# Optimization experiments

Hardware: AMD Instinct MI355X
Metric: run time of the kernel (lower is better)

## Reference

```python
import jax, jax.numpy as jnp
import numpy as np

B, S, K = 256, 50, 8
D, NH, NL = 512, 8, 2
N_KNOWS, N_PROBS = 1000, 20000
L2 = 2 * NL  # forward layers then backward layers, stacked
HD = D // NH
NEG = -1e9


def _ln(x, g, b, eps=1e-5):
    mu = x.mean(-1, keepdims=True)
    v = ((x - mu) ** 2).mean(-1, keepdims=True)
    return (x - mu) * jax.lax.rsqrt(v + eps) * g + b


def _block(x, m, Wq, bq, Wk, bk, Wv, bv, g1, be1, W1, b1, W2, b2, g2, be2):
    # x: [3B,S,D], m: [3B,1,S,S] additive-OR mask (True = blocked)
    Bx, Sx, Dx = x.shape
    Q = (x @ Wq + bq).reshape(Bx, Sx, NH, HD)
    Kt = (x @ Wk + bk).reshape(Bx, Sx, NH, HD)
    V = (x @ Wv + bv).reshape(Bx, Sx, NH, HD)
    a = jnp.einsum('bqnh,bknh->bnqk', Q, Kt) * (HD ** -0.5)
    a = jnp.where(m, NEG, a)
    p = jax.nn.softmax(a, axis=-1)
    p = jnp.where(m, 0.0, p)  # masked_fill + softmax + where, as in torch source
    o = jnp.einsum('bnqk,bknh->bqnh', p, V).reshape(Bx, Sx, Dx)
    x = _ln(x + o, g1, be1)
    h = jnp.maximum(x @ W1 + b1, 0.0) @ W2 + b2
    return _ln(x + h, g2, be2)


def _forward(probs_his, knows_his, corrs_his, knows_tab, probs_tab, types_tab, pos_tab,
             Wq, bq, Wk, bk, Wv, bv, g1, be1, W1, b1, W2, b2, g2, be2,
             pW1, pb1, pW2, pb2, pW3, pb3):
    info = knows_tab[knows_his].sum(-2) + probs_tab[probs_his] + pos_tab[jnp.arange(S)][None]
    c = corrs_his
    right_t = jnp.where(c, 1, 2)   # corrs==False -> 2
    wrong_t = jnp.where(c, 2, 0)   # corrs==True  -> 2
    norm_t = c.astype(jnp.int32)
    # fold the 3 counterfactual passes (right / wrong / normal) into the batch dim
    x3 = jnp.concatenate([info + types_tab[right_t], info + types_tab[wrong_t], info + types_tab[norm_t]], 0)
    kpm = jnp.tile(probs_his == 0, (3, 1))               # key padding mask [3B,S]
    km = kpm[:, :, None] | kpm[:, None, :]               # OR-combined [3B,S,S]
    tri = jnp.triu(jnp.ones((S, S), bool), 1)
    fm = (tri[None] | km)[:, None]                       # forward (causal) mask
    bm = (tri.T[None] | km)[:, None]                     # backward (anti-causal) mask
    f = x3
    b = x3
    for i in range(NL):
        f = _block(f, fm, Wq[i], bq[i], Wk[i], bk[i], Wv[i], bv[i], g1[i], be1[i], W1[i], b1[i], W2[i], b2[i], g2[i], be2[i])
    for i in range(NL, L2):
        b = _block(b, bm, Wq[i], bq[i], Wk[i], bk[i], Wv[i], bv[i], g1[i], be1[i], W1[i], b1[i], W2[i], b2[i], g2[i], be2[i])
    out = jnp.concatenate([b[:, :1], f[:, :-2] + b[:, 2:], f[:, -1:]], 1)
    h = jnp.concatenate([out, jnp.tile(info, (3, 1, 1))], -1)
    h = jnp.maximum(h @ pW1 + pb1, 0.0)
    h = jnp.maximum(h @ pW2 + pb2, 0.0)
    sc = jax.nn.sigmoid((h @ pW3 + pb3)[..., 0]).reshape(3, B, S)
    # zero out padded positions instead of ragged boolean gather (fixed shape, jit-safe)
    return jnp.where((probs_his > 0)[None], sc, 0.0)


def setup_inputs() -> dict:
    key = jax.random.key(0)
    ks = jax.random.split(key, 16)
    sc = 0.02
    d = {}
    d['probs_his'] = jax.random.randint(ks[0], (B, S), 0, N_PROBS)
    d['knows_his'] = jax.random.randint(ks[1], (B, S, K), 0, N_KNOWS + 1)
    d['corrs_his'] = jax.random.randint(ks[2], (B, S), 0, 2).astype(bool)
    d['knows_tab'] = (jax.random.normal(ks[3], (N_KNOWS + 1, D)) * sc).at[0].set(0.0)  # padding_idx=0
    d['probs_tab'] = (jax.random.normal(ks[4], (N_PROBS + 1, D)) * sc).at[0].set(0.0)
    d['types_tab'] = jax.random.normal(ks[5], (3, D)) * sc
    d['pos_tab'] = jax.random.normal(ks[6], (50, D)) * sc
    d['Wq'] = jax.random.normal(ks[7], (L2, D, D)) * sc
    d['Wk'] = jax.random.normal(ks[8], (L2, D, D)) * sc
    d['Wv'] = jax.random.normal(ks[9], (L2, D, D)) * sc
    d['W1'] = jax.random.normal(ks[10], (L2, D, D)) * sc
    d['W2'] = jax.random.normal(ks[11], (L2, D, D)) * sc
    for n in ('bq', 'bk', 'bv', 'b1', 'b2', 'be1', 'be2'):
        d[n] = jnp.zeros((L2, D))
    d['g1'] = jnp.ones((L2, D))
    d['g2'] = jnp.ones((L2, D))
    d['pW1'] = jax.random.normal(ks[12], (2 * D, D)) * sc
    d['pb1'] = jnp.zeros((D,))
    d['pW2'] = jax.random.normal(ks[13], (D, D // 2)) * sc
    d['pb2'] = jnp.zeros((D // 2,))
    d['pW3'] = jax.random.normal(ks[14], (D // 2, 1)) * sc
    d['pb3'] = jnp.zeros((1,))
    return d


def reference(probs_his, knows_his, corrs_his, knows_tab, probs_tab, types_tab, pos_tab,
              Wq, bq, Wk, bk, Wv, bv, g1, be1, W1, b1, W2, b2, g2, be2,
              pW1, pb1, pW2, pb2, pW3, pb3):
    return _forward(probs_his, knows_his, corrs_his, knows_tab, probs_tab, types_tab, pos_tab,
                    Wq, bq, Wk, bk, Wv, bv, g1, be1, W1, b1, W2, b2, g2, be2,
                    pW1, pb1, pW2, pb2, pW3, pb3)
```

## Files before the change

### kernel.cpp

```cpp
#include <hip/hip_runtime.h>
#include <hip/hip_bf16.h>

#define SEQ 50
#define DD  512
#define NHD 8
#define HDIM 64
#define MPROWS 38400
#define MTROWS 76800

typedef __hip_bfloat16 bf;
typedef __attribute__((ext_vector_type(8))) short bf16x8;
typedef __attribute__((ext_vector_type(4))) float f32x4;

__device__ __forceinline__ float bf2f(unsigned short u) {
    unsigned int x = ((unsigned int)u) << 16;
    return __builtin_bit_cast(float, x);
}
__device__ __forceinline__ unsigned short f2bu(float f) {
    unsigned int u = __builtin_bit_cast(unsigned int, f);
    u += 0x7fffu + ((u >> 16) & 1u);
    return (unsigned short)(u >> 16);
}

#define ASYNC16(g, l) __builtin_amdgcn_global_load_lds( \
    (__attribute__((address_space(1))) void*)(g),       \
    (__attribute__((address_space(3))) void*)(l), 16, 0, 0)

__global__ __launch_bounds__(256) void transpose_cast(
    const float* __restrict__ src, bf* __restrict__ dst,
    int R, int C, size_t sStride, size_t dStride)
{
    __shared__ float tile[32][33];
    int l = blockIdx.z;
    src += (size_t)l * sStride;
    dst += (size_t)l * dStride;
    int c0 = blockIdx.x * 32, r0 = blockIdx.y * 32;
    int tx = threadIdx.x & 31, ty = threadIdx.x >> 5;
    for (int i = ty; i < 32; i += 8)
        tile[i][tx] = src[(size_t)(r0 + i) * C + c0 + tx];
    __syncthreads();
    for (int i = ty; i < 32; i += 8)
        dst[(size_t)(c0 + i) * R + r0 + tx] = __float2bfloat16(tile[tx][i]);
}

__global__ __launch_bounds__(256) void biascat_kernel(
    const float* __restrict__ bq, const float* __restrict__ bk,
    const float* __restrict__ bv, float* __restrict__ out)
{
    int i = blockIdx.x * 256 + threadIdx.x;
    if (i >= 4 * 1536) return;
    int l = i / 1536, c = i % 1536;
    float v;
    if (c < 512)       v = bq[l * 512 + c];
    else if (c < 1024) v = bk[l * 512 + c - 512];
    else               v = bv[l * 512 + c - 1024];
    out[i] = v;
}

__global__ __launch_bounds__(256) void tproj_kernel(
    const float* __restrict__ types_tab, const bf* __restrict__ WTqkv,
    bf* __restrict__ Tt)
{
    int gid = blockIdx.x * 256 + threadIdx.x;
    if (gid >= 9216) return;
    int hl = gid / 4608;
    int t  = (gid / 1536) % 3;
    int n  = gid % 1536;
    const unsigned short* w =
        (const unsigned short*)(WTqkv + (size_t)(hl * 2) * 786432 + (size_t)n * 512);
    const float* ty = types_tab + t * 512;
    float a = 0.f;
    for (int k = 0; k < 512; ++k) a += ty[k] * bf2f(w[k]);
    Tt[gid] = __float2bfloat16(a);
}

__global__ __launch_bounds__(256) void embed_kernel(
    const int* __restrict__ probs_his, const int* __restrict__ knows_his,
    const int* __restrict__ corrs, const float* __restrict__ knows_tab,
    const float* __restrict__ probs_tab, const float* __restrict__ types_tab,
    const float* __restrict__ pos_tab, bf* __restrict__ info, bf* __restrict__ X)
{
    int bs = blockIdx.x * 4 + (threadIdx.x >> 6);
    int lane = threadIdx.x & 63;
    int s = bs % SEQ;
    int p = probs_his[bs];
    int c = corrs[bs];
    int d0 = lane * 8;

    float v[8];
    #pragma unroll
    for (int j = 0; j < 8; ++j)
        v[j] = probs_tab[(size_t)p * DD + d0 + j] + pos_tab[(size_t)s * DD + d0 + j];
    for (int k = 0; k < 8; ++k) {
        int ki = knows_his[bs * 8 + k];
        const float* kr = knows_tab + (size_t)ki * DD + d0;
        #pragma unroll
        for (int j = 0; j < 8; ++j) v[j] += kr[j];
    }
    int t0 = c ? 1 : 2;
    int t1 = c ? 2 : 0;
    int t2 = c ? 1 : 0;
    const float* T0 = types_tab + t0 * DD + d0;
    const float* T1 = types_tab + t1 * DD + d0;
    const float* T2 = types_tab + t2 * DD + d0;
    uint4 xi, x0, x1, x2;
    unsigned short* pi = (unsigned short*)&xi;
    unsigned short* p0 = (unsigned short*)&x0;
    unsigned short* p1 = (unsigned short*)&x1;
    unsigned short* p2 = (unsigned short*)&x2;
    #pragma unroll
    for (int j = 0; j < 8; ++j) {
        pi[j] = f2bu(v[j]);
        p0[j] = f2bu(v[j] + T0[j]);
        p1[j] = f2bu(v[j] + T1[j]);
        p2[j] = f2bu(v[j] + T2[j]);
    }
    size_t base = (size_t)bs * DD + d0;
    const size_t PB = (size_t)12800 * DD;
    *(uint4*)(info + base) = xi;
    *(uint4*)(X + 0 * PB + base) = x0;
    *(uint4*)(X + 1 * PB + base) = x1;
    *(uint4*)(X + 2 * PB + base) = x2;
    *(uint4*)(X + 3 * PB + base) = x0;
    *(uint4*)(X + 4 * PB + base) = x1;
    *(uint4*)(X + 5 * PB + base) = x2;
}

template <int RELU>
__global__ __launch_bounds__(256) void gemm_bt(
    const bf* __restrict__ Ap, const bf* __restrict__ WT0, const bf* __restrict__ WT1,
    const float* __restrict__ bias0, const float* __restrict__ bias1,
    bf* __restrict__ Cp, int N, int Kd, int nN, int mtHalf)
{
    __shared__ bf Al[128 * 64];
    __shared__ bf Bl[128 * 64];
    int nwg = gridDim.x;
    int f = blockIdx.x;
    int q8 = nwg >> 3, r8 = nwg & 7;
    int xcd = f & 7, pos = f >> 3;
    int e = (xcd < r8 ? xcd * (q8 + 1) : r8 * (q8 + 1) + (xcd - r8) * q8) + pos;
    int bm = e / nN, bn = e - bm * nN;
    const bf* WTp;
    const float* bias;
    if (bm < mtHalf) { WTp = WT0; bias = bias0; }
    else             { WTp = WT1; bias = bias1; }
    int m0 = bm * 128, n0 = bn * 128;
    int t = threadIdx.x, lane = t & 63, wave = t >> 6;
    int wr = wave >> 1, wc = wave & 1;
    int lr = lane & 15, lg = lane >> 4;

    f32x4 acc[4][4];
    #pragma unroll
    for (int m = 0; m < 4; ++m)
        #pragma unroll
        for (int n = 0; n < 4; ++n)
            acc[m][n] = (f32x4){0.f, 0.f, 0.f, 0.f};

    for (int kt = 0; kt < Kd; kt += 64) {
        #pragma unroll
        for (int i = 0; i < 4; ++i) {
            int c = i * 256 + t;
            int row = c >> 3, col = (c & 7) * 8;
            ASYNC16(Ap  + (size_t)(m0 + row) * Kd + kt + col, Al + c * 8);
            ASYNC16(WTp + (size_t)(n0 + row) * Kd + kt + col, Bl + c * 8);
        }
        __syncthreads();
        #pragma unroll
        for (int kk = 0; kk < 64; kk += 32) {
            int ko = kk + lg * 8;
            bf16x8 af[4], bfr[4];
            #pragma unroll
            for (int m = 0; m < 4; ++m)
                af[m] = *(const bf16x8*)(Al + (wr * 64 + m * 16 + lr) * 64 + ko);
            #pragma unroll
            for (int n = 0; n < 4; ++n)
                bfr[n] = *(const bf16x8*)(Bl + (wc * 64 + n * 16 + lr) * 64 + ko);
            #pragma unroll
            for (int m = 0; m < 4; ++m)
                #pragma unroll
                for (int n = 0; n < 4; ++n)
                    acc[m][n] = __builtin_amdgcn_mfma_f32_16x16x32_bf16(af[m], bfr[n], acc[m][n], 0, 0, 0);
        }
        __syncthreads();
    }
    unsigned short* Cs = (unsigned short*)Cp;
    #pragma unroll
    for (int n = 0; n < 4; ++n) {
        int col = n0 + wc * 64 + n * 16 + lr;
        float bvv = bias[col];
        #pragma unroll
        for (int m = 0; m < 4; ++m) {
            #pragma unroll
            for (int r = 0; r < 4; ++r) {
                int row = m0 + wr * 64 + m * 16 + lg * 4 + r;
                float v = acc[m][n][r] + bvv;
                if (RELU) v = fmaxf(v, 0.f);
                Cs[(size_t)row * N + col] = f2bu(v);
            }
        }
    }
}

__global__ __launch_bounds__(256) void gemm_l0(
    const bf* __restrict__ Ap, const bf* __restrict__ WTp,
    const float* __restrict__ bias, const bf* __restrict__ Tth,
    const int* __restrict__ corrs, bf* __restrict__ QKVc)
{
    __shared__ bf Al[128 * 64];
    __shared__ bf Bl[128 * 64];
    const int nN = 12, Kd = 512, N = 1536;
    int nwg = gridDim.x;
    int f = blockIdx.x;
    int q8 = nwg >> 3, r8 = nwg & 7;
    int xcd = f & 7, pos = f >> 3;
    int e = (xcd < r8 ? xcd * (q8 + 1) : r8 * (q8 + 1) + (xcd - r8) * q8) + pos;
    int bm = e / nN, bn = e - bm * nN;
    int m0 = bm * 128, n0 = bn * 128;
    int t = threadIdx.x, lane = t & 63, wave = t >> 6;
    int wr = wave >> 1, wc = wave & 1;
    int lr = lane & 15, lg = lane >> 4;

    f32x4 acc[4][4];
    #pragma unroll
    for (int m = 0; m < 4; ++m)
        #pragma unroll
        for (int n = 0; n < 4; ++n)
            acc[m][n] = (f32x4){0.f, 0.f, 0.f, 0.f};

    for (int kt = 0; kt < Kd; kt += 64) {
        #pragma unroll
        for (int i = 0; i < 4; ++i) {
            int c = i * 256 + t;
            int row = c >> 3, col = (c & 7) * 8;
            ASYNC16(Ap  + (size_t)(m0 + row) * Kd + kt + col, Al + c * 8);
            ASYNC16(WTp + (size_t)(n0 + row) * Kd + kt + col, Bl + c * 8);
        }
        __syncthreads();
        #pragma unroll
        for (int kk = 0; kk < 64; kk += 32) {
            int ko = kk + lg * 8;
            bf16x8 af[4], bfr[4];
            #pragma unroll
            for (int m = 0; m < 4; ++m)
                af[m] = *(const bf16x8*)(Al + (wr * 64 + m * 16 + lr) * 64 + ko);
            #pragma unroll
            for (int n = 0; n < 4; ++n)
                bfr[n] = *(const bf16x8*)(Bl + (wc * 64 + n * 16 + lr) * 64 + ko);
            #pragma unroll
            for (int m = 0; m < 4; ++m)
                #pragma unroll
                for (int n = 0; n < 4; ++n)
                    acc[m][n] = __builtin_amdgcn_mfma_f32_16x16x32_bf16(af[m], bfr[n], acc[m][n], 0, 0, 0);
        }
        __syncthreads();
    }
    unsigned short* Cs = (unsigned short*)QKVc;
    const unsigned short* Tu = (const unsigned short*)Tth;
    #pragma unroll
    for (int n = 0; n < 4; ++n) {
        int col = n0 + wc * 64 + n * 16 + lr;
        float bvv = bias[col];
        float T0c = bf2f(Tu[0 * 1536 + col]);
        float T1c = bf2f(Tu[1 * 1536 + col]);
        float T2c = bf2f(Tu[2 * 1536 + col]);
        #pragma unroll
        for (int m = 0; m < 4; ++m) {
            #pragma unroll
            for (int r = 0; r < 4; ++r) {
                int row = m0 + wr * 64 + m * 16 + lg * 4 + r;
                int c = corrs[row];
                float v = acc[m][n][r] + bvv;
                float tv0 = c ? T1c : T2c;
                float tv1 = c ? T2c : T0c;
                float tv2 = c ? T1c : T0c;
                size_t b0 = (size_t)row * N + col;
                Cs[b0]                         = f2bu(v + tv0);
                Cs[b0 + (size_t)12800 * N]     = f2bu(v + tv1);
                Cs[b0 + (size_t)25600 * N]     = f2bu(v + tv2);
            }
        }
    }
}

__global__ __launch_bounds__(256) void gemm_head(
    const bf* __restrict__ Ap, const bf* __restrict__ WTp,
    const bf* __restrict__ IPp, bf* __restrict__ Cp, int nN)
{
    __shared__ bf Al[128 * 64];
    __shared__ bf Bl[128 * 64];
    const int Kd = 512, N = 512;
    int nwg = gridDim.x;
    int f = blockIdx.x;
    int q8 = nwg >> 3, r8 = nwg & 7;
    int xcd = f & 7, pos = f >> 3;
    int e = (xcd < r8 ? xcd * (q8 + 1) : r8 * (q8 + 1) + (xcd - r8) * q8) + pos;
    int bm = e / nN, bn = e - bm * nN;
    int m0 = bm * 128, n0 = bn * 128;
    int t = threadIdx.x, lane = t & 63, wave = t >> 6;
    int wr = wave >> 1, wc = wave & 1;
    int lr = lane & 15, lg = lane >> 4;

    f32x4 acc[4][4];
    #pragma unroll
    for (int m = 0; m < 4; ++m)
        #pragma unroll
        for (int n = 0; n < 4; ++n)
            acc[m][n] = (f32x4){0.f, 0.f, 0.f, 0.f};

    for (int kt = 0; kt < Kd; kt += 64) {
        #pragma unroll
        for (int i = 0; i < 4; ++i) {
            int c = i * 256 + t;
            int row = c >> 3, col = (c & 7) * 8;
            ASYNC16(Ap  + (size_t)(m0 + row) * Kd + kt + col, Al + c * 8);
            ASYNC16(WTp + (size_t)(n0 + row) * Kd + kt + col, Bl + c * 8);
        }
        __syncthreads();
        #pragma unroll
        for (int kk = 0; kk < 64; kk += 32) {
            int ko = kk + lg * 8;
            bf16x8 af[4], bfr[4];
            #pragma unroll
            for (int m = 0; m < 4; ++m)
                af[m] = *(const bf16x8*)(Al + (wr * 64 + m * 16 + lr) * 64 + ko);
            #pragma unroll
            for (int n = 0; n < 4; ++n)
                bfr[n] = *(const bf16x8*)(Bl + (wc * 64 + n * 16 + lr) * 64 + ko);
            #pragma unroll
            for (int m = 0; m < 4; ++m)
                #pragma unroll
                for (int n = 0; n < 4; ++n)
                    acc[m][n] = __builtin_amdgcn_mfma_f32_16x16x32_bf16(af[m], bfr[n], acc[m][n], 0, 0, 0);
        }
        __syncthreads();
    }
    unsigned short* Cs = (unsigned short*)Cp;
    const unsigned short* IPu = (const unsigned short*)IPp;
    #pragma unroll
    for (int n = 0; n < 4; ++n) {
        int col = n0 + wc * 64 + n * 16 + lr;
        #pragma unroll
        for (int m = 0; m < 4; ++m) {
            #pragma unroll
            for (int r = 0; r < 4; ++r) {
                int row = m0 + wr * 64 + m * 16 + lg * 4 + r;
                int rr = row % 12800;
                float v = acc[m][n][r] + bf2f(IPu[(size_t)rr * 512 + col]);
                v = fmaxf(v, 0.f);
                Cs[(size_t)row * N + col] = f2bu(v);
            }
        }
    }
}

__global__ __launch_bounds__(128, 2) void attn_mfma(
    const bf* __restrict__ QKVc, const int* __restrict__ probs_his,
    bf* __restrict__ Oc, int seq0)
{
    __shared__ bf Pl_s[2][4096];
    __shared__ bf Vt_s[2][4096];
    int wave = threadIdx.x >> 6, lane = threadIdx.x & 63;
    bf* Pl = Pl_s[wave];
    bf* Vt = Vt_s[wave];
    int task = blockIdx.x * 2 + wave;
    int h = task & 7, seqL = task >> 3;
    int seqG = seq0 + seqL;
    int st = seqG / 768, b = seqG % 256;
    int lr = lane & 15, kg = lane >> 4;
    const bf* Qb = QKVc + (size_t)seqL * SEQ * 1536 + h * HDIM;
    const bf* Kb = Qb + 512;
    const bf* Vb = Qb + 1024;

    int pvv = (lane < SEQ) ? probs_his[b * SEQ + lane] : 1;
    unsigned long long padm = __ballot(pvv == 0) | 0xFFFC000000000000ull;

    #pragma unroll
    for (int it = 0; it < 8; ++it) {
        int idx = it * 64 + lane;
        int key = idx >> 3, d0 = (idx & 7) * 8;
        uint4 v4 = make_uint4(0u, 0u, 0u, 0u);
        if (key < SEQ) v4 = *(const uint4*)(Vb + (size_t)key * 1536 + d0);
        unsigned short* vs = (unsigned short*)&v4;
        #pragma unroll
        for (int j = 0; j < 8; ++j) {
            int d = d0 + j;
            int byt = (d * 128 + key * 2) ^ ((j & 7) << 4);
            *(unsigned short*)((char*)Vt + byt) = vs[j];
        }
    }

    bf16x8 kf[4][2], qf[4][2];
    #pragma unroll
    for (int m = 0; m < 4; ++m) {
        int rk = 16 * m + lr; if (rk > SEQ - 1) rk = SEQ - 1;
        #pragma unroll
        for (int kb = 0; kb < 2; ++kb) {
            kf[m][kb] = *(const bf16x8*)(Kb + (size_t)rk * 1536 + kb * 32 + kg * 8);
            qf[m][kb] = *(const bf16x8*)(Qb + (size_t)rk * 1536 + kb * 32 + kg * 8);
        }
    }
    f32x4 sacc[4][4];
    #pragma unroll
    for (int m = 0; m < 4; ++m)
        #pragma unroll
        for (int n = 0; n < 4; ++n)
            sacc[m][n] = (f32x4){0.f, 0.f, 0.f, 0.f};
    #pragma unroll
    for (int kb = 0; kb < 2; ++kb)
        #pragma unroll
        for (int m = 0; m < 4; ++m)
            #pragma unroll
            for (int n = 0; n < 4; ++n)
                sacc[m][n] = __builtin_amdgcn_mfma_f32_16x16x32_bf16(kf[m][kb], qf[n][kb], sacc[m][n], 0, 0, 0);

    #pragma unroll
    for (int n = 0; n < 4; ++n) {
        int q = 16 * n + lr;
        int qpad = (int)((padm >> q) & 1ull);
        float p[4][4];
        float mx = -3e38f;
        #pragma unroll
        for (int m = 0; m < 4; ++m)
            #pragma unroll
            for (int r = 0; r < 4; ++r) {
                int key = 16 * m + 4 * kg + r;
                int blocked = qpad | (int)((padm >> key) & 1ull) |
                              (st == 0 ? (key > q) : (key < q));
                float s = sacc[m][n][r] * 0.125f;
                p[m][r] = blocked ? -3e38f : s;
                if (!blocked) mx = fmaxf(mx, s);
            }
        mx = fmaxf(mx, __shfl_xor(mx, 16));
        mx = fmaxf(mx, __shfl_xor(mx, 32));
        float sum = 0.f;
        #pragma unroll
        for (int m = 0; m < 4; ++m)
            #pragma unroll
            for (int r = 0; r < 4; ++r) {
                float e = (p[m][r] > -1e37f) ? __expf(p[m][r] - mx) : 0.f;
                p[m][r] = e;
                sum += e;
            }
        sum += __shfl_xor(sum, 16);
        sum += __shfl_xor(sum, 32);
        float inv = (sum > 0.f) ? 1.f / sum : 0.f;
        #pragma unroll
        for (int m = 0; m < 4; ++m) {
            unsigned int u0 = (unsigned int)f2bu(p[m][0] * inv) |
                              ((unsigned int)f2bu(p[m][1] * inv) << 16);
            unsigned int u1 = (unsigned int)f2bu(p[m][2] * inv) |
                              ((unsigned int)f2bu(p[m][3] * inv) << 16);
            int base = (q * 128 + (16 * m + 4 * kg) * 2) ^ ((q & 7) << 4);
            *(unsigned int*)((char*)Pl + base) = u0;
            *(unsigned int*)((char*)Pl + base + 4) = u1;
        }
    }

    f32x4 oacc[4][4];
    #pragma unroll
    for (int m = 0; m < 4; ++m)
        #pragma unroll
        for (int n = 0; n < 4; ++n)
            oacc[m][n] = (f32x4){0.f, 0.f, 0.f, 0.f};
    #pragma unroll
    for (int kb = 0; kb < 2; ++kb) {
        bf16x8 vf[4], pf[4];
        #pragma unroll
        for (int m = 0; m < 4; ++m) {
            int row = 16 * m + lr;
            int byt = (row * 128 + (kb * 32 + kg * 8) * 2) ^ ((row & 7) << 4);
            vf[m] = *(const bf16x8*)((char*)Vt + byt);
            pf[m] = *(const bf16x8*)((char*)Pl + byt);
        }
        #pragma unroll
        for (int m = 0; m < 4; ++m)
            #pragma unroll
            for (int n = 0; n < 4; ++n)
                oacc[m][n] = __builtin_amdgcn_mfma_f32_16x16x32_bf16(vf[m], pf[n], oacc[m][n], 0, 0, 0);
    }

    #pragma unroll
    for (int n = 0; n < 4; ++n) {
        int q = 16 * n + lr;
        if (q < SEQ) {
            #pragma unroll
            for (int m = 0; m < 4; ++m) {
                uint2 ov;
                ov.x = (unsigned int)f2bu(oacc[m][n][0]) | ((unsigned int)f2bu(oacc[m][n][1]) << 16);
                ov.y = (unsigned int)f2bu(oacc[m][n][2]) | ((unsigned int)f2bu(oacc[m][n][3]) << 16);
                *(uint2*)(Oc + (size_t)(seqL * SEQ + q) * DD + h * HDIM + 16 * m + 4 * kg) = ov;
            }
        }
    }
}

__global__ __launch_bounds__(256) void ln_kernel(
    bf* __restrict__ X, const bf* __restrict__ Rb,
    const float* __restrict__ g_all, const float* __restrict__ be_all,
    int lf, int lb)
{
    int row = blockIdx.x * 4 + (threadIdx.x >> 6);
    int lane = threadIdx.x & 63;
    int layer = (row < MPROWS) ? lf : lb;
    const float* g = g_all + layer * DD;
    const float* be = be_all + layer * DD;
    uint4 xa = *((const uint4*)(X + (size_t)row * DD) + lane);
    uint4 ra = *((const uint4*)(Rb + (size_t)row * DD) + lane);
    unsigned short* xs = (unsigned short*)&xa;
    unsigned short* rs = (unsigned short*)&ra;
    float v[8];
    float sum = 0.f;
    #pragma unroll
    for (int j = 0; j < 8; ++j) { v[j] = bf2f(xs[j]) + bf2f(rs[j]); sum += v[j]; }
    #pragma unroll
    for (int o = 1; o < 64; o <<= 1) sum += __shfl_xor(sum, o);
    float mu = sum * (1.f / 512.f);
    float ss = 0.f;
    #pragma unroll
    for (int j = 0; j < 8; ++j) { float d = v[j] - mu; ss += d * d; }
    #pragma unroll
    for (int o = 1; o < 64; o <<= 1) ss += __shfl_xor(ss, o);
    float inv = rsqrtf(ss * (1.f / 512.f) + 1e-5f);
    int d0 = lane * 8;
    uint4 ov;
    unsigned short* os = (unsigned short*)&ov;
    #pragma unroll
    for (int j = 0; j < 8; ++j)
        os[j] = f2bu((v[j] - mu) * inv * g[d0 + j] + be[d0 + j]);
    *((uint4*)(X + (size_t)row * DD) + lane) = ov;
}

__global__ __launch_bounds__(256) void combine_kernel(
    const bf* __restrict__ X, const bf* __restrict__ info,
    bf* __restrict__ Hinc, int rh0, int hstride, int withInfo)
{
    int rl = blockIdx.x * 4 + (threadIdx.x >> 6);
    int rh = rh0 + rl;
    int lane = threadIdx.x & 63;
    int s = rh % SEQ, pb = rh / SEQ, b = pb & 255;
    const size_t MPD = (size_t)MPROWS * DD;
    uint4 o;
    if (s == 0) {
        o = *((const uint4*)(X + MPD + (size_t)(pb * SEQ) * DD) + lane);
    } else if (s == SEQ - 1) {
        o = *((const uint4*)(X + (size_t)(pb * SEQ + SEQ - 1) * DD) + lane);
    } else {
        uint4 a = *((const uint4*)(X + (size_t)(pb * SEQ + s - 1) * DD) + lane);
        uint4 c2 = *((const uint4*)(X + MPD + (size_t)(pb * SEQ + s + 1) * DD) + lane);
        unsigned short* as = (unsigned short*)&a;
        unsigned short* cs = (unsigned short*)&c2;
        unsigned short* os = (unsigned short*)&o;
        #pragma unroll
        for (int j = 0; j < 8; ++j) os[j] = f2bu(bf2f(as[j]) + bf2f(cs[j]));
    }
    *((uint4*)(Hinc + (size_t)rl * hstride) + lane) = o;
    if (withInfo) {
        uint4 iv = *((const uint4*)(info + (size_t)(b * SEQ + s) * DD) + lane);
        *((uint4*)(Hinc + (size_t)rl * hstride + 512) + lane) = iv;
    }
}

__global__ __launch_bounds__(256) void head_final(
    const bf* __restrict__ h2c, const float* __restrict__ pW3,
    const float* __restrict__ pb3, const int* __restrict__ probs_his,
    float* __restrict__ out, int rh0)
{
    int rl = blockIdx.x * 4 + (threadIdx.x >> 6);
    int row = rh0 + rl;
    int lane = threadIdx.x & 63;
    uint2 hv = *((const uint2*)(h2c + (size_t)rl * 256) + lane);
    unsigned short* hs = (unsigned short*)&hv;
    float s = 0.f;
    #pragma unroll
    for (int j = 0; j < 4; ++j) s += bf2f(hs[j]) * pW3[lane * 4 + j];
    #pragma unroll
    for (int o = 1; o < 64; o <<= 1) s += __shfl_xor(s, o);
    if (lane == 0) {
        float logit = s + pb3[0];
        float sc = 1.f / (1.f + __expf(-logit));
        int bb = (row / SEQ) & 255, ss2 = row % SEQ;
        out[row] = (probs_his[bb * SEQ + ss2] > 0) ? sc : 0.f;
    }
}

extern "C" void kernel_launch(void* const* d_in, const int* in_sizes, int n_in,
                              void* d_out, int out_size, void* d_ws, size_t ws_size,
                              hipStream_t stream) {
    const int*   probs_his = (const int*)d_in[0];
    const int*   knows_his = (const int*)d_in[1];
    const int*   corrs     = (const int*)d_in[2];
    const float* knows_tab = (const float*)d_in[3];
    const float* probs_tab = (const float*)d_in[4];
    const float* types_tab = (const float*)d_in[5];
    const float* pos_tab   = (const float*)d_in[6];
    const float* Wq = (const float*)d_in[7];
    const float* Wk = (const float*)d_in[8];
    const float* Wv = (const float*)d_in[9];
    const float* W1 = (const float*)d_in[10];
    const float* W2 = (const float*)d_in[11];
    const float* bq = (const float*)d_in[12];
    const float* bk = (const float*)d_in[13];
    const float* bv = (const float*)d_in[14];
    const float* b1 = (const float*)d_in[15];
    const float* b2 = (const float*)d_in[16];
    const float* be1 = (const float*)d_in[17];
    const float* be2 = (const float*)d_in[18];
    const float* g1 = (const float*)d_in[19];
    const float* g2 = (const float*)d_in[20];
    const float* pW1 = (const float*)d_in[21];
    const float* pb1 = (const float*)d_in[22];
    const float* pW2 = (const float*)d_in[23];
    const float* pb2 = (const float*)d_in[24];
    const float* pW3 = (const float*)d_in[25];
    const float* pb3 = (const float*)d_in[26];

    char* ws = (char*)d_ws;
    bf* WTqkv = (bf*)(ws + 0);
    bf* WT1   = (bf*)(ws + 6291456);
    bf* WT2   = (bf*)(ws + 8388608);
    bf* pW1T  = (bf*)(ws + 10485760);
    bf* pW1aT = (bf*)(ws + 11534336);
    bf* pW1bT = (bf*)(ws + 12058624);
    bf* pW2T  = (bf*)(ws + 12582912);
    float* bqkv = (float*)(ws + 12845056);
    bf* info  = (bf*)(ws + 12869632);
    bf* X     = (bf*)(ws + 25976832);
    const size_t FIXED = 104620032ull;
    const size_t FULLSCR = (size_t)38400 * 4096;

    int CR;
    if      (ws_size >= FIXED + FULLSCR)                  CR = 38400;
    else if (ws_size >= FIXED + (size_t)19200 * 4096)     CR = 19200;
    else if (ws_size >= FIXED + (size_t)9600  * 4096)     CR = 9600;
    else                                                  CR = 3200;
    const int full = (CR == 38400) &&
        (ws_size >= FIXED + FULLSCR + 18432);
    bf* Tt = (bf*)(ws + FIXED + FULLSCR);

    char* SCR = ws + FIXED;

    biascat_kernel<<<dim3(24), dim3(256), 0, stream>>>(bq, bk, bv, bqkv);
    transpose_cast<<<dim3(16,16,4), dim3(256), 0, stream>>>(Wq, WTqkv,          512, 512, 262144, 786432);
    transpose_cast<<<dim3(16,16,4), dim3(256), 0, stream>>>(Wk, WTqkv + 262144, 512, 512, 262144, 786432);
    transpose_cast<<<dim3(16,16,4), dim3(256), 0, stream>>>(Wv, WTqkv + 524288, 512, 512, 262144, 786432);
    transpose_cast<<<dim3(16,16,4), dim3(256), 0, stream>>>(W1, WT1, 512, 512, 262144, 262144);
    transpose_cast<<<dim3(16,16,4), dim3(256), 0, stream>>>(W2, WT2, 512, 512, 262144, 262144);
    transpose_cast<<<dim3(16,32,1), dim3(256), 0, stream>>>(pW1, pW1T, 1024, 512, 0, 0);
    transpose_cast<<<dim3(16,16,1), dim3(256), 0, stream>>>(pW1, pW1aT, 512, 512, 0, 0);
    transpose_cast<<<dim3(16,16,1), dim3(256), 0, stream>>>(pW1 + 262144, pW1bT, 512, 512, 0, 0);
    transpose_cast<<<dim3(8,16,1),  dim3(256), 0, stream>>>(pW2, pW2T, 512, 256, 0, 0);
    embed_kernel<<<dim3(3200), dim3(256), 0, stream>>>(probs_his, knows_his, corrs,
        knows_tab, probs_tab, types_tab, pos_tab, info, X);
    if (full)
        tproj_kernel<<<dim3(36), dim3(256), 0, stream>>>(types_tab, WTqkv, Tt);

    const int BIG = 1 << 30;

    if (full) {
        bf* QKVc = (bf*)SCR;
        bf* Oc   = (bf*)(SCR + (size_t)38400 * 3072);
        bf* F1c  = (bf*)SCR;
        bf* F2c  = (bf*)(SCR + (size_t)76800 * 1024);
        bf* Hin  = (bf*)SCR;
        bf* h1c  = (bf*)(SCR + 39321600);
        bf* h2c  = (bf*)(SCR + 78643200);
        bf* IPb  = (bf*)(SCR + 98304000);

        for (int i = 0; i < 2; ++i) {
            for (int hlf = 0; hlf < 2; ++hlf) {
                int lidx = i + 2 * hlf;
                bf* Xh = X + (size_t)hlf * 38400 * DD;
                if (i == 0) {
                    gemm_l0<<<dim3(1200), dim3(256), 0, stream>>>(
                        info, WTqkv + (size_t)lidx * 786432, bqkv + lidx * 1536,
                        Tt + hlf * 4608, corrs, QKVc);
                } else {
                    gemm_bt<0><<<dim3(3600), dim3(256), 0, stream>>>(
                        Xh, WTqkv + (size_t)lidx * 786432, WTqkv + (size_t)lidx * 786432,
                        bqkv + lidx * 1536, bqkv + lidx * 1536, QKVc, 1536, 512, 12, BIG);
                }
                attn_mfma<<<dim3(3072), dim3(128), 0, stream>>>(
                    QKVc, probs_his, Oc, hlf * 768);
                ln_kernel<<<dim3(9600), dim3(256), 0, stream>>>(
                    Xh, Oc, g1, be1, lidx, lidx);
            }
            gemm_bt<1><<<dim3(2400), dim3(256), 0, stream>>>(
                X, WT1 + (size_t)i * 262144, WT1 + (size_t)(i + 2) * 262144,
                b1 + i * 512, b1 + (i + 2) * 512, F1c, 512, 512, 4, 300);
            gemm_bt<0><<<dim3(2400), dim3(256), 0, stream>>>(
                F1c, WT2 + (size_t)i * 262144, WT2 + (size_t)(i + 2) * 262144,
                b2 + i * 512, b2 + (i + 2) * 512, F2c, 512, 512, 4, 300);
            ln_kernel<<<dim3(19200), dim3(256), 0, stream>>>(
                X, F2c, g2, be2, i, i + 2);
        }

        combine_kernel<<<dim3(9600), dim3(256), 0, stream>>>(X, info, Hin, 0, 512, 0);
        gemm_bt<0><<<dim3(400), dim3(256), 0, stream>>>(
            info, pW1bT, pW1bT, pb1, pb1, IPb, 512, 512, 4, BIG);
        gemm_head<<<dim3(1200), dim3(256), 0, stream>>>(Hin, pW1aT, IPb, h1c, 4);
        gemm_bt<1><<<dim3(600), dim3(256), 0, stream>>>(
            h1c, pW2T, pW2T, pb2, pb2, h2c, 256, 512, 2, BIG);
        head_final<<<dim3(9600), dim3(256), 0, stream>>>(
            h2c, pW3, pb3, probs_his, (float*)d_out, 0);
        return;
    }

    bf* QKVc = (bf*)SCR;
    bf* Oc   = (bf*)(SCR + (size_t)CR * 3072);
    bf* F1c  = (bf*)SCR;
    bf* F2c  = (bf*)(SCR + (size_t)CR * 1024);
    bf* Hinc = (bf*)SCR;
    bf* h1c  = (bf*)(SCR + (size_t)CR * 2048);
    bf* h2c  = (bf*)(SCR + (size_t)CR * 3072);

    const int nck = 38400 / CR;
    const int MT = CR / 128;
    for (int i = 0; i < 2; ++i) {
        for (int hlf = 0; hlf < 2; ++hlf) {
            int lidx = i + 2 * hlf;
            const bf* WTq  = WTqkv + (size_t)lidx * 786432;
            const bf* WT1l = WT1   + (size_t)lidx * 262144;
            const bf* WT2l = WT2   + (size_t)lidx * 262144;
            for (int c = 0; c < nck; ++c) {
                int r0 = hlf * 38400 + c * CR;
                gemm_bt<0><<<dim3(MT * 12), dim3(256), 0, stream>>>(
                    X + (size_t)r0 * DD, WTq, WTq, bqkv + lidx * 1536,
                    bqkv + lidx * 1536, QKVc, 1536, 512, 12, BIG);
                attn_mfma<<<dim3((CR/50) * 4), dim3(128), 0, stream>>>(
                    QKVc, probs_his, Oc, r0 / 50);
                ln_kernel<<<dim3(CR/4), dim3(256), 0, stream>>>(
                    X + (size_t)r0 * DD, Oc, g1, be1, lidx, lidx);
            }
            for (int c = 0; c < nck; ++c) {
                int r0 = hlf * 38400 + c * CR;
                gemm_bt<1><<<dim3(MT * 4), dim3(256), 0, stream>>>(
                    X + (size_t)r0 * DD, WT1l, WT1l, b1 + lidx * 512,
                    b1 + lidx * 512, F1c, 512, 512, 4, BIG);
                gemm_bt<0><<<dim3(MT * 4), dim3(256), 0, stream>>>(
                    F1c, WT2l, WT2l, b2 + lidx * 512, b2 + lidx * 512,
                    F2c, 512, 512, 4, BIG);
                ln_kernel<<<dim3(CR/4), dim3(256), 0, stream>>>(
                    X + (size_t)r0 * DD, F2c, g2, be2, lidx, lidx);
            }
        }
    }
    for (int c = 0; c < nck; ++c) {
        int rh0 = c * CR;
        combine_kernel<<<dim3(CR/4), dim3(256), 0, stream>>>(X, info, Hinc, rh0, 1024, 1);
        gemm_bt<1><<<dim3(MT * 4), dim3(256), 0, stream>>>(
            Hinc, pW1T, pW1T, pb1, pb1, h1c, 512, 1024, 4, BIG);
        gemm_bt<1><<<dim3(MT * 2), dim3(256), 0, stream>>>(
            h1c, pW2T, pW2T, pb2, pb2, h2c, 256, 512, 2, BIG);
        head_final<<<dim3(CR/4), dim3(256), 0, stream>>>(
            h2c, pW3, pb3, probs_his, (float*)d_out, rh0);
    }
}
```

Measured before the change: 1.155 ms.

## Fuse attention with residual LayerNorm and FFN2 GEMM with residual LayerNorm

Adds an attn_ln kernel: one 512-thread block per sequence, one wave per head. It computes attention and then the residual add plus LayerNorm, reducing row statistics across heads through shared memory. It also adds ffn2_ln, a 64x512 full-row-tile GEMM that applies bias, residual and LayerNorm in its epilogue. The separate attention-output and FFN2-output buffers and both ln_kernel launches go away, saving a round trip through global memory per layer. In exchange, attn_ln asks for 128KB of LDS per block, so occupancy is one block per CU. The wide GEMM tile has fewer blocks and no double buffering, which may lower GEMM efficiency.

```diff
diff --git a/kernel.cpp b/kernel.cpp
--- a/kernel.cpp
+++ b/kernel.cpp
@@ -274,9 +274,9 @@
                 float tv1 = c ? T2c : T0c;
                 float tv2 = c ? T1c : T0c;
                 size_t b0 = (size_t)row * N + col;
-                Cs[b0]                         = f2bu(v + tv0);
-                Cs[b0 + (size_t)12800 * N]     = f2bu(v + tv1);
-                Cs[b0 + (size_t)25600 * N]     = f2bu(v + tv2);
+                Cs[b0]                     = f2bu(v + tv0);
+                Cs[b0 + (size_t)12800 * N] = f2bu(v + tv1);
+                Cs[b0 + (size_t)25600 * N] = f2bu(v + tv2);
             }
         }
     }
@@ -353,6 +353,306 @@
     }
 }
 
+__global__ __launch_bounds__(512, 1) void attn_ln(
+    const bf* __restrict__ QKVc, const int* __restrict__ probs_his,
+    bf* __restrict__ Xh, const float* __restrict__ g, const float* __restrict__ be,
+    int seq0)
+{
+    __shared__ char smem[131072];
+    int wave = threadIdx.x >> 6, lane = threadIdx.x & 63;
+    bf* Pl = (bf*)(smem + wave * 16384);
+    bf* Vt = (bf*)(smem + wave * 16384 + 8192);
+    float (*part)[64][2] = (float(*)[64][2])smem;
+    int h = wave;
+    int seqL = blockIdx.x;
+    int seqG = seq0 + seqL;
+    int st = seqG / 768, b = seqG % 256;
+    int lr = lane & 15, kg = lane >> 4;
+    const bf* Qb = QKVc + (size_t)seqL * SEQ * 1536 + h * HDIM;
+    const bf* Kb = Qb + 512;
+    const bf* Vb = Qb + 1024;
+
+    int pvv = (lane < SEQ) ? probs_his[b * SEQ + lane] : 1;
+    unsigned long long padm = __ballot(pvv == 0) | 0xFFFC000000000000ull;
+
+    #pragma unroll
+    for (int it = 0; it < 8; ++it) {
+        int idx = it * 64 + lane;
+        int key = idx >> 3, d0 = (idx & 7) * 8;
+        uint4 v4 = make_uint4(0u, 0u, 0u, 0u);
+        if (key < SEQ) v4 = *(const uint4*)(Vb + (size_t)key * 1536 + d0);
+        unsigned short* vs = (unsigned short*)&v4;
+        #pragma unroll
+        for (int j = 0; j < 8; ++j) {
+            int d = d0 + j;
+            int byt = (d * 128 + key * 2) ^ ((j & 7) << 4);
+            *(unsigned short*)((char*)Vt + byt) = vs[j];
+        }
+    }
+
+    bf16x8 kf[4][2], qf[4][2];
+    #pragma unroll
+    for (int m = 0; m < 4; ++m) {
+        int rk = 16 * m + lr; if (rk > SEQ - 1) rk = SEQ - 1;
+        #pragma unroll
+        for (int kb = 0; kb < 2; ++kb) {
+            kf[m][kb] = *(const bf16x8*)(Kb + (size_t)rk * 1536 + kb * 32 + kg * 8);
+            qf[m][kb] = *(const bf16x8*)(Qb + (size_t)rk * 1536 + kb * 32 + kg * 8);
+        }
+    }
+    f32x4 sacc[4][4];
+    #pragma unroll
+    for (int m = 0; m < 4; ++m)
+        #pragma unroll
+        for (int n = 0; n < 4; ++n)
+            sacc[m][n] = (f32x4){0.f, 0.f, 0.f, 0.f};
+    #pragma unroll
+    for (int kb = 0; kb < 2; ++kb)
+        #pragma unroll
+        for (int m = 0; m < 4; ++m)
+            #pragma unroll
+            for (int n = 0; n < 4; ++n)
+                sacc[m][n] = __builtin_amdgcn_mfma_f32_16x16x32_bf16(kf[m][kb], qf[n][kb], sacc[m][n], 0, 0, 0);
+
+    #pragma unroll
+    for (int n = 0; n < 4; ++n) {
+        int q = 16 * n + lr;
+        int qpad = (int)((padm >> q) & 1ull);
+        float p[4][4];
+        float mx = -3e38f;
+        #pragma unroll
+        for (int m = 0; m < 4; ++m)
+            #pragma unroll
+            for (int r = 0; r < 4; ++r) {
+                int key = 16 * m + 4 * kg + r;
+                int blocked = qpad | (int)((padm >> key) & 1ull) |
+                              (st == 0 ? (key > q) : (key < q));
+                float s = sacc[m][n][r] * 0.125f;
+                p[m][r] = blocked ? -3e38f : s;
+                if (!blocked) mx = fmaxf(mx, s);
+            }
+        mx = fmaxf(mx, __shfl_xor(mx, 16));
+        mx = fmaxf(mx, __shfl_xor(mx, 32));
+        float sum = 0.f;
+        #pragma unroll
+        for (int m = 0; m < 4; ++m)
+            #pragma unroll
+            for (int r = 0; r < 4; ++r) {
+                float e = (p[m][r] > -1e37f) ? __expf(p[m][r] - mx) : 0.f;
+                p[m][r] = e;
+                sum += e;
+            }
+        sum += __shfl_xor(sum, 16);
+        sum += __shfl_xor(sum, 32);
+        float inv = (sum > 0.f) ? 1.f / sum : 0.f;
+        #pragma unroll
+        for (int m = 0; m < 4; ++m) {
+            unsigned int u0 = (unsigned int)f2bu(p[m][0] * inv) |
+                              ((unsigned int)f2bu(p[m][1] * inv) << 16);
+            unsigned int u1 = (unsigned int)f2bu(p[m][2] * inv) |
+                              ((unsigned int)f2bu(p[m][3] * inv) << 16);
+            int base = (q * 128 + (16 * m + 4 * kg) * 2) ^ ((q & 7) << 4);
+            *(unsigned int*)((char*)Pl + base) = u0;
+            *(unsigned int*)((char*)Pl + base + 4) = u1;
+        }
+    }
+
+    f32x4 oacc[4][4];
+    #pragma unroll
+    for (int m = 0; m < 4; ++m)
+        #pragma unroll
+        for (int n = 0; n < 4; ++n)
+            oacc[m][n] = (f32x4){0.f, 0.f, 0.f, 0.f};
+    #pragma unroll
+    for (int kb = 0; kb < 2; ++kb) {
+        bf16x8 vf[4], pf[4];
+        #pragma unroll
+        for (int m = 0; m < 4; ++m) {
+            int row = 16 * m + lr;
+            int byt = (row * 128 + (kb * 32 + kg * 8) * 2) ^ ((row & 7) << 4);
+            vf[m] = *(const bf16x8*)((char*)Vt + byt);
+            pf[m] = *(const bf16x8*)((char*)Pl + byt);
+        }
+        #pragma unroll
+        for (int m = 0; m < 4; ++m)
+            #pragma unroll
+            for (int n = 0; n < 4; ++n)
+                oacc[m][n] = __builtin_amdgcn_mfma_f32_16x16x32_bf16(vf[m], pf[n], oacc[m][n], 0, 0, 0);
+    }
+
+    uint2 xr[4][4];
+    float ps[4], pss[4];
+    #pragma unroll
+    for (int n = 0; n < 4; ++n) {
+        int q = 16 * n + lr;
+        float s = 0.f, ss = 0.f;
+        #pragma unroll
+        for (int m = 0; m < 4; ++m) {
+            uint2 xv = make_uint2(0u, 0u);
+            if (q < SEQ)
+                xv = *(const uint2*)(Xh + (size_t)(seqL * SEQ + q) * DD + h * HDIM + 16 * m + 4 * kg);
+            xr[n][m] = xv;
+            unsigned short* xs = (unsigned short*)&xv;
+            #pragma unroll
+            for (int r = 0; r < 4; ++r) {
+                float v = oacc[m][n][r] + bf2f(xs[r]);
+                s += v; ss += v * v;
+            }
+        }
+        s += __shfl_xor(s, 16); s += __shfl_xor(s, 32);
+        ss += __shfl_xor(ss, 16); ss += __shfl_xor(ss, 32);
+        ps[n] = s; pss[n] = ss;
+    }
+    __syncthreads();
+    #pragma unroll
+    for (int n = 0; n < 4; ++n) {
+        int q = 16 * n + lr;
+        if (kg == 0) { part[h][q][0] = ps[n]; part[h][q][1] = pss[n]; }
+    }
+    __syncthreads();
+
+    #pragma unroll
+    for (int n = 0; n < 4; ++n) {
+        int q = 16 * n + lr;
+        if (q >= SEQ) continue;
+        float s = 0.f, ss = 0.f;
+        #pragma unroll
+        for (int hh = 0; hh < 8; ++hh) { s += part[hh][q][0]; ss += part[hh][q][1]; }
+        float mu = s * (1.f / 512.f);
+        float inv = rsqrtf(ss * (1.f / 512.f) - mu * mu + 1e-5f);
+        #pragma unroll
+        for (int m = 0; m < 4; ++m) {
+            unsigned short* xs = (unsigned short*)&xr[n][m];
+            uint2 ov;
+            unsigned short* os = (unsigned short*)&ov;
+            #pragma unroll
+            for (int r = 0; r < 4; ++r) {
+                int col = h * HDIM + 16 * m + 4 * kg + r;
+                float v = oacc[m][n][r] + bf2f(xs[r]);
+                os[r] = f2bu((v - mu) * inv * g[col] + be[col]);
+            }
+            *(uint2*)(Xh + (size_t)(seqL * SEQ + q) * DD + h * HDIM + 16 * m + 4 * kg) = ov;
+        }
+    }
+}
+
+__global__ __launch_bounds__(256, 2) void ffn2_ln(
+    const bf* __restrict__ F1, const bf* __restrict__ WT0, const bf* __restrict__ WT1,
+    const float* __restrict__ b20, const float* __restrict__ b21,
+    const float* __restrict__ g20, const float* __restrict__ g21,
+    const float* __restrict__ be20, const float* __restrict__ be21,
+    bf* __restrict__ Xp, int mtHalf)
+{
+    __shared__ bf Al[64 * 64];
+    __shared__ bf Bl[512 * 64];
+    __shared__ float part[4][64][2];
+    int bm = blockIdx.x;
+    const bf* WTp; const float *b2, *g2, *be2;
+    if (bm < mtHalf) { WTp = WT0; b2 = b20; g2 = g20; be2 = be20; }
+    else             { WTp = WT1; b2 = b21; g2 = g21; be2 = be21; }
+    int m0 = bm * 64;
+    int t = threadIdx.x, lane = t & 63, wave = t >> 6;
+    int lr = lane & 15, lg = lane >> 4;
+
+    f32x4 acc[4][8];
+    #pragma unroll
+    for (int m = 0; m < 4; ++m)
+        #pragma unroll
+        for (int n = 0; n < 8; ++n)
+            acc[m][n] = (f32x4){0.f, 0.f, 0.f, 0.f};
+
+    for (int kt = 0; kt < 512; kt += 64) {
+        #pragma unroll
+        for (int i = 0; i < 2; ++i) {
+            int c = i * 256 + t;
+            int row = c >> 3, col = (c & 7) * 8;
+            ASYNC16(F1 + (size_t)(m0 + row) * 512 + kt + col, Al + c * 8);
+        }
+        #pragma unroll
+        for (int i = 0; i < 16; ++i) {
+            int c = i * 256 + t;
+            int row = c >> 3, col = (c & 7) * 8;
+            ASYNC16(WTp + (size_t)row * 512 + kt + col, Bl + c * 8);
+        }
+        __syncthreads();
+        #pragma unroll
+        for (int kk = 0; kk < 64; kk += 32) {
+            int ko = kk + lg * 8;
+            bf16x8 af[4], bfr[8];
+            #pragma unroll
+            for (int m = 0; m < 4; ++m)
+                af[m] = *(const bf16x8*)(Al + (m * 16 + lr) * 64 + ko);
+            #pragma unroll
+            for (int n = 0; n < 8; ++n)
+                bfr[n] = *(const bf16x8*)(Bl + (wave * 128 + n * 16 + lr) * 64 + ko);
+            #pragma unroll
+            for (int m = 0; m < 4; ++m)
+                #pragma unroll
+                for (int n = 0; n < 8; ++n)
+                    acc[m][n] = __builtin_amdgcn_mfma_f32_16x16x32_bf16(af[m], bfr[n], acc[m][n], 0, 0, 0);
+        }
+        __syncthreads();
+    }
+
+    #pragma unroll
+    for (int i = 0; i < 16; ++i) {
+        int c = i * 256 + t;
+        int row = c >> 6, ch = c & 63;
+        int sw = (row ^ (row >> 2)) & 7;
+        int colsrc = (ch ^ sw) * 8;
+        ASYNC16(Xp + (size_t)(m0 + row) * 512 + colsrc, Bl + c * 8);
+    }
+    __syncthreads();
+    const unsigned short* Xl = (const unsigned short*)Bl;
+
+    float bv[8], gv[8], bev[8];
+    #pragma unroll
+    for (int n = 0; n < 8; ++n) {
+        int col = wave * 128 + n * 16 + lr;
+        bv[n] = b2[col]; gv[n] = g2[col]; bev[n] = be2[col];
+    }
+#define XLD(row, col) bf2f(Xl[(row) * 512 + ((((((col) >> 3) ^ (((row) ^ ((row) >> 2)) & 7))) << 3) | ((col) & 7))])
+    #pragma unroll
+    for (int m = 0; m < 4; ++m) {
+        #pragma unroll
+        for (int r = 0; r < 4; ++r) {
+            int row = m * 16 + lg * 4 + r;
+            float s = 0.f, ss = 0.f;
+            #pragma unroll
+            for (int n = 0; n < 8; ++n) {
+                int col = wave * 128 + n * 16 + lr;
+                float v = acc[m][n][r] + bv[n] + XLD(row, col);
+                s += v; ss += v * v;
+            }
+            s += __shfl_xor(s, 1); s += __shfl_xor(s, 2);
+            s += __shfl_xor(s, 4); s += __shfl_xor(s, 8);
+            ss += __shfl_xor(ss, 1); ss += __shfl_xor(ss, 2);
+            ss += __shfl_xor(ss, 4); ss += __shfl_xor(ss, 8);
+            if (lr == 0) { part[wave][row][0] = s; part[wave][row][1] = ss; }
+        }
+    }
+    __syncthreads();
+    unsigned short* Xs = (unsigned short*)Xp;
+    #pragma unroll
+    for (int m = 0; m < 4; ++m) {
+        #pragma unroll
+        for (int r = 0; r < 4; ++r) {
+            int row = m * 16 + lg * 4 + r;
+            float s  = part[0][row][0] + part[1][row][0] + part[2][row][0] + part[3][row][0];
+            float ss = part[0][row][1] + part[1][row][1] + part[2][row][1] + part[3][row][1];
+            float mu = s * (1.f / 512.f);
+            float inv = rsqrtf(ss * (1.f / 512.f) - mu * mu + 1e-5f);
+            #pragma unroll
+            for (int n = 0; n < 8; ++n) {
+                int col = wave * 128 + n * 16 + lr;
+                float v = acc[m][n][r] + bv[n] + XLD(row, col);
+                Xs[(size_t)(m0 + row) * 512 + col] = f2bu((v - mu) * inv * gv[n] + bev[n]);
+            }
+        }
+    }
+#undef XLD
+}
+
 __global__ __launch_bounds__(128, 2) void attn_mfma(
     const bf* __restrict__ QKVc, const int* __restrict__ probs_his,
     bf* __restrict__ Oc, int seq0)
@@ -478,7 +778,6 @@
             for (int n = 0; n < 4; ++n)
                 oacc[m][n] = __builtin_amdgcn_mfma_f32_16x16x32_bf16(vf[m], pf[n], oacc[m][n], 0, 0, 0);
     }
-
     #pragma unroll
     for (int n = 0; n < 4; ++n) {
         int q = 16 * n + lr;
@@ -658,9 +957,7 @@
 
     if (full) {
         bf* QKVc = (bf*)SCR;
-        bf* Oc   = (bf*)(SCR + (size_t)38400 * 3072);
         bf* F1c  = (bf*)SCR;
-        bf* F2c  = (bf*)(SCR + (size_t)76800 * 1024);
         bf* Hin  = (bf*)SCR;
         bf* h1c  = (bf*)(SCR + 39321600);
         bf* h2c  = (bf*)(SCR + 78643200);
@@ -679,19 +976,17 @@
                         Xh, WTqkv + (size_t)lidx * 786432, WTqkv + (size_t)lidx * 786432,
                         bqkv + lidx * 1536, bqkv + lidx * 1536, QKVc, 1536, 512, 12, BIG);
                 }
-                attn_mfma<<<dim3(3072), dim3(128), 0, stream>>>(
-                    QKVc, probs_his, Oc, hlf * 768);
-                ln_kernel<<<dim3(9600), dim3(256), 0, stream>>>(
-                    Xh, Oc, g1, be1, lidx, lidx);
+                attn_ln<<<dim3(768), dim3(512), 0, stream>>>(
+                    QKVc, probs_his, Xh, g1 + lidx * DD, be1 + lidx * DD, hlf * 768);
             }
             gemm_bt<1><<<dim3(2400), dim3(256), 0, stream>>>(
                 X, WT1 + (size_t)i * 262144, WT1 + (size_t)(i + 2) * 262144,
                 b1 + i * 512, b1 + (i + 2) * 512, F1c, 512, 512, 4, 300);
-            gemm_bt<0><<<dim3(2400), dim3(256), 0, stream>>>(
+            ffn2_ln<<<dim3(1200), dim3(256), 0, stream>>>(
                 F1c, WT2 + (size_t)i * 262144, WT2 + (size_t)(i + 2) * 262144,
-                b2 + i * 512, b2 + (i + 2) * 512, F2c, 512, 512, 4, 300);
-            ln_kernel<<<dim3(19200), dim3(256), 0, stream>>>(
-                X, F2c, g2, be2, i, i + 2);
+                b2 + i * 512, b2 + (i + 2) * 512,
+                g2 + i * 512, g2 + (i + 2) * 512,
+                be2 + i * 512, be2 + (i + 2) * 512, X, 600);
         }
 
         combine_kernel<<<dim3(9600), dim3(256), 0, stream>>>(X, info, Hin, 0, 512, 0);
```

Result: no change. 1.169 ms (+1.2%).

## Add 256x256-tile double-buffered GEMM for layer-1 QKV projection

Applied to the files above, without the earlier changes.

Introduces a new GEMM kernel with 512 threads, 256x256 output tiles, double-buffered LDS staging via async global-to-LDS loads, and interleaved prefetch across four sub-steps with MFMA priority bumps. It replaces the 128x128-tile kernel for the second-layer QKV projection. The aim is to raise arithmetic intensity per workgroup and overlap global loads with MFMA work. The larger tile uses 128 KB of LDS and many accumulator registers, which may limit occupancy. Only 900 workgroups are launched, which may leave some compute units idle in the tail.

```diff
diff --git a/kernel.cpp b/kernel.cpp
--- a/kernel.cpp
+++ b/kernel.cpp
@@ -201,6 +201,121 @@
     }
 }
 
+template <int RELU>
+__global__ __launch_bounds__(512, 2) void gemm8(
+    const bf* __restrict__ Ap, const bf* __restrict__ WTp,
+    const float* __restrict__ bias, bf* __restrict__ Cp,
+    int N, int Kd, int nN)
+{
+    __shared__ __align__(16) bf As[2][16384];
+    __shared__ __align__(16) bf Bs[2][16384];
+
+    int nwg = gridDim.x, f = blockIdx.x;
+    int q8 = nwg >> 3, r8 = nwg & 7;
+    int xcd = f & 7, pos = f >> 3;
+    int e = (xcd < r8 ? xcd * (q8 + 1) : r8 * (q8 + 1) + (xcd - r8) * q8) + pos;
+    int bm = e / nN, bn = e - bm * nN;
+    int m0 = bm * 256, n0 = bn * 256;
+    int t = threadIdx.x, lane = t & 63, wave = t >> 6;
+    int wm = wave >> 2, wn = wave & 3;
+    int lr = lane & 15, kg = lane >> 4;
+
+    int srow = t >> 3;
+    int scolb = (t & 7) * 16;
+    const bf* Abase = Ap + (size_t)m0 * Kd;
+    const bf* Bbase = WTp + (size_t)n0 * Kd;
+
+#define STG(dsts, base, half, kt) do {                                        \
+    _Pragma("unroll")                                                         \
+    for (int _i = 0; _i < 2; ++_i) {                                          \
+        int _r = (half) * 128 + _i * 64 + srow;                               \
+        ASYNC16((base) + (size_t)_r * Kd + (kt) +                             \
+                    ((scolb ^ ((_r & 7) << 4)) >> 1),                         \
+                (dsts) + _r * 64 + (t & 7) * 8);                              \
+    } } while (0)
+
+    f32x4 acc[8][4];
+    #pragma unroll
+    for (int m = 0; m < 8; ++m)
+        #pragma unroll
+        for (int n = 0; n < 4; ++n)
+            acc[m][n] = (f32x4){0.f, 0.f, 0.f, 0.f};
+
+    STG(As[0], Abase, 0, 0);
+    STG(As[0], Abase, 1, 0);
+    STG(Bs[0], Bbase, 0, 0);
+    STG(Bs[0], Bbase, 1, 0);
+
+    int ntile = Kd >> 6;
+    bf16x8 breg[4][2];
+    for (int j = 0; j < ntile; ++j) {
+        int d = j & 1;
+        const char* Ab = (const char*)As[d];
+        const char* Bb = (const char*)Bs[d];
+        asm volatile("s_waitcnt vmcnt(0)" ::: "memory");
+        __builtin_amdgcn_s_barrier();
+        int kt1 = (j + 1) << 6;
+        int pf = (j + 1 < ntile);
+        #pragma unroll
+        for (int q = 0; q < 4; ++q) {
+            if (q == 0) {
+                #pragma unroll
+                for (int ns = 0; ns < 4; ++ns) {
+                    int row = wn * 64 + ns * 16 + lr;
+                    int sw = (row & 7) << 4;
+                    breg[ns][0] = *(const bf16x8*)(Bb + row * 128 + ((kg * 16) ^ sw));
+                    breg[ns][1] = *(const bf16x8*)(Bb + row * 128 + ((64 + kg * 16) ^ sw));
+                }
+            }
+            bf16x8 areg[2][2];
+            #pragma unroll
+            for (int mm = 0; mm < 2; ++mm) {
+                int row = wm * 128 + (2 * q + mm) * 16 + lr;
+                int sw = (row & 7) << 4;
+                areg[mm][0] = *(const bf16x8*)(Ab + row * 128 + ((kg * 16) ^ sw));
+                areg[mm][1] = *(const bf16x8*)(Ab + row * 128 + ((64 + kg * 16) ^ sw));
+            }
+            if (pf) {
+                if (q == 0)      STG(As[d ^ 1], Abase, 0, kt1);
+                else if (q == 1) STG(As[d ^ 1], Abase, 1, kt1);
+                else if (q == 2) STG(Bs[d ^ 1], Bbase, 0, kt1);
+                else             STG(Bs[d ^ 1], Bbase, 1, kt1);
+            }
+            __builtin_amdgcn_s_barrier();
+            __builtin_amdgcn_s_setprio(1);
+            #pragma unroll
+            for (int mm = 0; mm < 2; ++mm)
+                #pragma unroll
+                for (int ns = 0; ns < 4; ++ns) {
+                    acc[2 * q + mm][ns] = __builtin_amdgcn_mfma_f32_16x16x32_bf16(
+                        areg[mm][0], breg[ns][0], acc[2 * q + mm][ns], 0, 0, 0);
+                    acc[2 * q + mm][ns] = __builtin_amdgcn_mfma_f32_16x16x32_bf16(
+                        areg[mm][1], breg[ns][1], acc[2 * q + mm][ns], 0, 0, 0);
+                }
+            __builtin_amdgcn_s_setprio(0);
+            if (q != 3) __builtin_amdgcn_s_barrier();
+        }
+    }
+#undef STG
+
+    unsigned short* Cs = (unsigned short*)Cp;
+    #pragma unroll
+    for (int ns = 0; ns < 4; ++ns) {
+        int col = n0 + wn * 64 + ns * 16 + lr;
+        float bvv = bias[col];
+        #pragma unroll
+        for (int ms = 0; ms < 8; ++ms) {
+            #pragma unroll
+            for (int rr = 0; rr < 4; ++rr) {
+                int row = m0 + wm * 128 + ms * 16 + kg * 4 + rr;
+                float v = acc[ms][ns][rr] + bvv;
+                if (RELU) v = fmaxf(v, 0.f);
+                Cs[(size_t)row * N + col] = f2bu(v);
+            }
+        }
+    }
+}
+
 __global__ __launch_bounds__(256) void gemm_l0(
     const bf* __restrict__ Ap, const bf* __restrict__ WTp,
     const float* __restrict__ bias, const bf* __restrict__ Tth,
@@ -274,9 +389,9 @@
                 float tv1 = c ? T2c : T0c;
                 float tv2 = c ? T1c : T0c;
                 size_t b0 = (size_t)row * N + col;
-                Cs[b0]                         = f2bu(v + tv0);
-                Cs[b0 + (size_t)12800 * N]     = f2bu(v + tv1);
-                Cs[b0 + (size_t)25600 * N]     = f2bu(v + tv2);
+                Cs[b0]                     = f2bu(v + tv0);
+                Cs[b0 + (size_t)12800 * N] = f2bu(v + tv1);
+                Cs[b0 + (size_t)25600 * N] = f2bu(v + tv2);
             }
         }
     }
@@ -478,7 +593,6 @@
             for (int n = 0; n < 4; ++n)
                 oacc[m][n] = __builtin_amdgcn_mfma_f32_16x16x32_bf16(vf[m], pf[n], oacc[m][n], 0, 0, 0);
     }
-
     #pragma unroll
     for (int n = 0; n < 4; ++n) {
         int q = 16 * n + lr;
@@ -675,9 +789,9 @@
                         info, WTqkv + (size_t)lidx * 786432, bqkv + lidx * 1536,
                         Tt + hlf * 4608, corrs, QKVc);
                 } else {
-                    gemm_bt<0><<<dim3(3600), dim3(256), 0, stream>>>(
-                        Xh, WTqkv + (size_t)lidx * 786432, WTqkv + (size_t)lidx * 786432,
-                        bqkv + lidx * 1536, bqkv + lidx * 1536, QKVc, 1536, 512, 12, BIG);
+                    gemm8<0><<<dim3(900), dim3(512), 0, stream>>>(
+                        Xh, WTqkv + (size_t)lidx * 786432, bqkv + lidx * 1536,
+                        QKVc, 1536, 512, 6);
                 }
                 attn_mfma<<<dim3(3072), dim3(128), 0, stream>>>(
                     QKVc, probs_his, Oc, hlf * 768);
```

Measured after the change: 1.123 ms. -2.8%, faster.
